# Performance work log

Measured on AMD Instinct MI355X. Metric: run time of the kernel, lower is better.

The kernel has to match this reference:

```python
import jax, jax.numpy as jnp
import numpy as np

D_MODEL = 1024
NUM_HEADS = 16
DEPTH = D_MODEL // NUM_HEADS


def setup_inputs() -> dict:
    key = jax.random.key(0)
    ks = jax.random.split(key, 6)
    B, S = 2, 2048
    scale = 1.0 / np.sqrt(D_MODEL)
    return {
        "q": jax.random.normal(ks[0], (B, S, D_MODEL), jnp.float32),
        "k": jax.random.normal(ks[1], (B, S, D_MODEL), jnp.float32),
        "v": jax.random.normal(ks[2], (B, S, D_MODEL), jnp.float32),
        "wq": jax.random.normal(ks[3], (D_MODEL, D_MODEL), jnp.float32) * scale,
        "wk": jax.random.normal(ks[4], (D_MODEL, D_MODEL), jnp.float32) * scale,
        "wv": jax.random.normal(ks[5], (D_MODEL, D_MODEL), jnp.float32) * scale,
    }


def reference(q, k, v, wq, wk, wv):
    B, S, _ = q.shape
    # Linear projections (nn.Linear: x @ W.T), then split heads -> [B,H,S,depth]
    def split(x):
        return x.reshape(B, -1, NUM_HEADS, DEPTH).transpose(0, 2, 1, 3)
    Q = split(q @ wq.T)
    K = split(k @ wk.T)
    V = split(v @ wv.T)
    scores = jnp.einsum("bhqd,bhkd->bhqk", Q, K) / np.sqrt(DEPTH).astype(np.float32)
    attn = jax.nn.softmax(scores, axis=-1)
    out = jnp.einsum("bhqk,bhkd->bhqd", attn, V)
    # merge heads; note: original forward never applies self.dense
    return out.transpose(0, 2, 1, 3).reshape(B, S, D_MODEL)
```

## Files before the change

kernel.cpp:

```cpp
#include <hip/hip_runtime.h>
#include <hip/hip_bf16.h>
#include <stdint.h>

#define B_SZ 2
#define S_LEN 2048
#define DM 1024
#define NH 16
#define DEPTH 64
#define M_ROWS (B_SZ * S_LEN)
#define SCALE_Q 0.1803368801111144f

typedef __attribute__((ext_vector_type(8))) short bf16x8;
typedef __attribute__((ext_vector_type(4))) float f32x4;
typedef __attribute__((ext_vector_type(16))) float f32x16;

__device__ __forceinline__ unsigned short f2bf(float x) {
    union { float f; unsigned u; } a; a.f = x;
    unsigned r = a.u + 0x7FFF + ((a.u >> 16) & 1);
    return (unsigned short)(r >> 16);
}

__device__ __forceinline__ void async_ld16(const unsigned short* g, void* l) {
    __builtin_amdgcn_global_load_lds(
        (const __attribute__((address_space(1))) void*)g,
        (__attribute__((address_space(3))) void*)l,
        16, 0, 0);
}


__global__ __launch_bounds__(256)
void convert_kernel(const float* __restrict__ q, const float* __restrict__ k,
                    const float* __restrict__ v, const float* __restrict__ wq,
                    const float* __restrict__ wk, const float* __restrict__ wv,
                    unsigned short* __restrict__ dst) {
    const int z = blockIdx.y;
    const float* src = (z == 0) ? q : (z == 1) ? k : (z == 2) ? v
                     : (z == 3) ? wq : (z == 4) ? wk : wv;
    const size_t n4  = (z < 3) ? ((size_t)M_ROWS * DM / 4) : ((size_t)DM * DM / 4);
    const size_t off = (z < 3) ? ((size_t)z * M_ROWS * DM)
                               : ((size_t)3 * M_ROWS * DM + (size_t)(z - 3) * DM * DM);
    unsigned short* d = dst + off;
    const size_t stride = (size_t)gridDim.x * blockDim.x;
    for (size_t i = (size_t)blockIdx.x * blockDim.x + threadIdx.x; i < n4; i += stride) {
        float4 x = ((const float4*)src)[i];
        ushort4 p;
        p.x = f2bf(x.x); p.y = f2bf(x.y); p.z = f2bf(x.z); p.w = f2bf(x.w);
        ((ushort4*)d)[i] = p;
    }
}

__global__ __launch_bounds__(256)
void proj_gemm3_kernel(const unsigned short* __restrict__ Xall,
                       const unsigned short* __restrict__ Wall,
                       unsigned short* __restrict__ Call) {
    __shared__ unsigned short As[128 * 64];
    __shared__ unsigned short Bs[128 * 64];

    const int z = blockIdx.z;
    const unsigned short* X = Xall + (size_t)z * M_ROWS * DM;
    const unsigned short* W = Wall + (size_t)z * DM * DM;
    unsigned short* C = Call + (size_t)z * M_ROWS * DM;

    const int tid  = threadIdx.x;
    const int wave = tid >> 6;
    const int lane = tid & 63;
    const int l32  = lane & 31;
    const int s    = lane >> 5;
    const int m0 = blockIdx.x * 128;
    const int n0 = blockIdx.y * 128;
    const int wm = (wave >> 1) * 64;
    const int wn = (wave & 1) * 64;

    const int r8 = lane >> 3;
    const int sc = (lane & 7) ^ r8;

    f32x16 acc[2][2];
#pragma unroll
    for (int mi = 0; mi < 2; ++mi)
#pragma unroll
        for (int ni = 0; ni < 2; ++ni)
#pragma unroll
            for (int r = 0; r < 16; ++r) acc[mi][ni][r] = 0.f;

    for (int k0 = 0; k0 < DM; k0 += 64) {
#pragma unroll
        for (int i = 0; i < 4; ++i) {
            const int r = i * 32 + wave * 8 + r8;
            async_ld16(X + (size_t)(m0 + r) * DM + k0 + sc * 8,
                       (char*)As + i * 4096 + wave * 1024);
            async_ld16(W + (size_t)(n0 + r) * DM + k0 + sc * 8,
                       (char*)Bs + i * 4096 + wave * 1024);
        }
        __syncthreads();

#pragma unroll
        for (int ch = 0; ch < 4; ++ch) {
            bf16x8 af[2], bfr[2];
#pragma unroll
            for (int mi = 0; mi < 2; ++mi) {
                const int row = wm + mi * 32 + l32;
                af[mi] = *(const bf16x8*)&As[row * 64 + (((2 * ch + s) ^ (row & 7)) * 8)];
            }
#pragma unroll
            for (int ni = 0; ni < 2; ++ni) {
                const int row = wn + ni * 32 + l32;
                bfr[ni] = *(const bf16x8*)&Bs[row * 64 + (((2 * ch + s) ^ (row & 7)) * 8)];
            }
#pragma unroll
            for (int mi = 0; mi < 2; ++mi)
#pragma unroll
                for (int ni = 0; ni < 2; ++ni)
                    acc[mi][ni] = __builtin_amdgcn_mfma_f32_32x32x16_bf16(
                        af[mi], bfr[ni], acc[mi][ni], 0, 0, 0);
        }
        __syncthreads();
    }

    const float scale = (z == 0) ? SCALE_Q : 1.0f;
#pragma unroll
    for (int mi = 0; mi < 2; ++mi)
#pragma unroll
        for (int ni = 0; ni < 2; ++ni)
#pragma unroll
            for (int r = 0; r < 16; ++r) {
                const int row = m0 + wm + mi * 32 + (r & 3) + 8 * (r >> 2) + 4 * s;
                const int col = n0 + wn + ni * 32 + l32;
                C[(size_t)row * DM + col] = f2bf(acc[mi][ni][r] * scale);
            }
}

__global__ __launch_bounds__(256)
void vtrans_kernel(const unsigned short* __restrict__ Vp,
                   unsigned short* __restrict__ Vt) {
    __shared__ unsigned short Ls[64 * 72];
    const int tr = blockIdx.x;
    const int h  = blockIdx.y;
    const int tid = threadIdx.x;

#pragma unroll
    for (int i = 0; i < 2; ++i) {
        const int id = i * 256 + tid;
        const int r = id >> 3, c = id & 7;
        bf16x8 v8 = *(const bf16x8*)&Vp[(size_t)(tr * 64 + r) * DM + h * 64 + c * 8];
        *(bf16x8*)&Ls[r * 72 + ((c ^ (r & 7)) * 8)] = v8;
    }
    __syncthreads();

    const int b = tr >> 5;
    const int col0 = (tr & 31) * 64;
#pragma unroll
    for (int i = 0; i < 2; ++i) {
        const int id = i * 256 + tid;
        const int d = id >> 3, c2 = id & 7;
        unsigned short tmp[8];
#pragma unroll
        for (int j = 0; j < 8; ++j) {
            const int cc = c2 * 8 + j;
            const int t = (cc >> 1) + ((cc & 1) << 5);
            tmp[j] = Ls[t * 72 + (((d >> 3) ^ (t & 7)) * 8) + (d & 7)];
        }
        *(bf16x8*)&Vt[(size_t)((b * NH + h) * DEPTH + d) * S_LEN + col0 + c2 * 8] =
            *(const bf16x8*)tmp;
    }
}

__global__ __launch_bounds__(256)
void attn3_kernel(const unsigned short* __restrict__ Qp,
                  const unsigned short* __restrict__ Kp,
                  const unsigned short* __restrict__ Vt,
                  float* __restrict__ out) {
    __shared__ unsigned short Ks[64 * 64];
    __shared__ unsigned short Vs[64 * 64];
    __shared__ unsigned short Ps[4 * 32 * 72];

    const int tid  = threadIdx.x;
    const int wave = tid >> 6;
    const int lane = tid & 63;
    const int l32  = lane & 31;
    const int s    = lane >> 5;
    const int q0 = blockIdx.x * 128;
    const int h  = blockIdx.y;
    const int b  = blockIdx.z;

    const int r8 = lane >> 3;
    const int sc = (lane & 7) ^ r8;

    const unsigned short* Kg = Kp + (size_t)(b * S_LEN) * DM + h * DEPTH;
    const unsigned short* Vg = Vt + (size_t)((b * NH + h) * DEPTH) * S_LEN;

    bf16x8 qf[4];
    {
        const unsigned short* p =
            Qp + (size_t)(b * S_LEN + q0 + wave * 32 + l32) * DM + h * DEPTH;
#pragma unroll
        for (int ch = 0; ch < 4; ++ch)
            qf[ch] = *(const bf16x8*)(p + ch * 16 + s * 8);
    }

    f32x16 oacc[2];
    float lacc[16];
#pragma unroll
    for (int d = 0; d < 2; ++d)
#pragma unroll
        for (int r = 0; r < 16; ++r) oacc[d][r] = 0.f;
#pragma unroll
    for (int r = 0; r < 16; ++r) lacc[r] = 0.f;

    unsigned short* PsW = &Ps[wave * 32 * 72];

    for (int t0 = 0; t0 < S_LEN; t0 += 64) {
#pragma unroll
        for (int i = 0; i < 2; ++i) {
            const int r = i * 32 + wave * 8 + r8;
            async_ld16(Kg + (size_t)(t0 + r) * DM + sc * 8,
                       (char*)Ks + i * 4096 + wave * 1024);
            async_ld16(Vg + (size_t)r * S_LEN + t0 + sc * 8,
                       (char*)Vs + i * 4096 + wave * 1024);
        }
        __syncthreads();

        f32x16 sacc[2];
#pragma unroll
        for (int tb = 0; tb < 2; ++tb) {
#pragma unroll
            for (int r = 0; r < 16; ++r) sacc[tb][r] = 0.f;
            const int trow = tb * 32 + l32;
#pragma unroll
            for (int ch = 0; ch < 4; ++ch) {
                bf16x8 kf = *(const bf16x8*)
                    &Ks[trow * 64 + (((2 * ch + s) ^ (trow & 7)) * 8)];
                sacc[tb] = __builtin_amdgcn_mfma_f32_32x32x16_bf16(
                    qf[ch], kf, sacc[tb], 0, 0, 0);
            }
        }

#pragma unroll
        for (int r = 0; r < 16; ++r) {
            const float p0 = __builtin_amdgcn_exp2f(sacc[0][r]);
            const float p1 = __builtin_amdgcn_exp2f(sacc[1][r]);
            union { float f; unsigned u; } a0, a1;
            a0.f = p0; a1.f = p1;
            union { unsigned u; float f; } t0f, t1f;
            t0f.u = a0.u & 0xFFFF0000u;
            t1f.u = a1.u & 0xFFFF0000u;
            lacc[r] += t0f.f + t1f.f;
            const unsigned pk = (a0.u >> 16) | (a1.u & 0xFFFF0000u);
            const int qrow = (r & 3) + 8 * (r >> 2) + 4 * s;
            *(unsigned*)&PsW[qrow * 72 + 2 * l32] = pk;
        }

        bf16x8 pf[4];
#pragma unroll
        for (int ch = 0; ch < 4; ++ch)
            pf[ch] = *(const bf16x8*)&PsW[l32 * 72 + ch * 16 + s * 8];
#pragma unroll
        for (int db = 0; db < 2; ++db) {
            const int drow = db * 32 + l32;
#pragma unroll
            for (int ch = 0; ch < 4; ++ch) {
                bf16x8 vf = *(const bf16x8*)
                    &Vs[drow * 64 + (((2 * ch + s) ^ (drow & 7)) * 8)];
                oacc[db] = __builtin_amdgcn_mfma_f32_32x32x16_bf16(
                    pf[ch], vf, oacc[db], 0, 0, 0);
            }
        }
        __syncthreads();
    }

#pragma unroll
    for (int r = 0; r < 16; ++r)
#pragma unroll
        for (int off = 1; off < 32; off <<= 1)
            lacc[r] += __shfl_xor(lacc[r], off, 64);

#pragma unroll
    for (int db = 0; db < 2; ++db)
#pragma unroll
        for (int r = 0; r < 16; ++r) {
            const int qrow = (r & 3) + 8 * (r >> 2) + 4 * s;
            const size_t row = (size_t)(b * S_LEN + q0 + wave * 32 + qrow);
            out[row * DM + h * DEPTH + db * 32 + l32] = oacc[db][r] / lacc[r];
        }
}

#define LDK 72

__global__ __launch_bounds__(256)
void proj_gemm_kernel(const float* __restrict__ q, const float* __restrict__ k,
                      const float* __restrict__ v, const float* __restrict__ wq,
                      const float* __restrict__ wk, const float* __restrict__ wv,
                      unsigned short* __restrict__ Qp, unsigned short* __restrict__ Kp,
                      unsigned short* __restrict__ Vp) {
    __shared__ unsigned short As[128 * LDK];
    __shared__ unsigned short Bs[128 * LDK];

    const int z = blockIdx.z;
    const float* __restrict__ X = (z == 0) ? q : (z == 1) ? k : v;
    const float* __restrict__ W = (z == 0) ? wq : (z == 1) ? wk : wv;
    unsigned short* __restrict__ C = (z == 0) ? Qp : (z == 1) ? Kp : Vp;

    const int tid  = threadIdx.x;
    const int wave = tid >> 6;
    const int lane = tid & 63;
    const int quad = lane >> 4;
    const int l16  = lane & 15;
    const int m0 = blockIdx.x * 128;
    const int n0 = blockIdx.y * 128;
    const int wm = (wave >> 1) * 64;
    const int wn = (wave & 1) * 64;

    f32x4 acc[4][4];
#pragma unroll
    for (int mt = 0; mt < 4; ++mt)
#pragma unroll
        for (int nt = 0; nt < 4; ++nt)
            acc[mt][nt] = (f32x4){0.f, 0.f, 0.f, 0.f};

    for (int k0 = 0; k0 < DM; k0 += 64) {
#pragma unroll
        for (int vv = 0; vv < 8; ++vv) {
            int vecid = tid + 256 * vv;
            int r  = vecid >> 4;
            int c4 = vecid & 15;
            const float4 xa = *(const float4*)&X[(size_t)(m0 + r) * DM + k0 + c4 * 4];
            ushort4 pa;
            pa.x = f2bf(xa.x); pa.y = f2bf(xa.y); pa.z = f2bf(xa.z); pa.w = f2bf(xa.w);
            *(ushort4*)&As[r * LDK + c4 * 4] = pa;
            const float4 xb = *(const float4*)&W[(size_t)(n0 + r) * DM + k0 + c4 * 4];
            ushort4 pb;
            pb.x = f2bf(xb.x); pb.y = f2bf(xb.y); pb.z = f2bf(xb.z); pb.w = f2bf(xb.w);
            *(ushort4*)&Bs[r * LDK + c4 * 4] = pb;
        }
        __syncthreads();

#pragma unroll
        for (int kc = 0; kc < 2; ++kc) {
            bf16x8 af[4], bfr[4];
#pragma unroll
            for (int mt = 0; mt < 4; ++mt)
                af[mt] = *(const bf16x8*)&As[(wm + mt * 16 + l16) * LDK + kc * 32 + quad * 8];
#pragma unroll
            for (int nt = 0; nt < 4; ++nt)
                bfr[nt] = *(const bf16x8*)&Bs[(wn + nt * 16 + l16) * LDK + kc * 32 + quad * 8];
#pragma unroll
            for (int mt = 0; mt < 4; ++mt)
#pragma unroll
                for (int nt = 0; nt < 4; ++nt)
                    acc[mt][nt] = __builtin_amdgcn_mfma_f32_16x16x32_bf16(
                        af[mt], bfr[nt], acc[mt][nt], 0, 0, 0);
        }
        __syncthreads();
    }

#pragma unroll
    for (int mt = 0; mt < 4; ++mt)
#pragma unroll
        for (int nt = 0; nt < 4; ++nt)
#pragma unroll
            for (int r = 0; r < 4; ++r) {
                int row = m0 + wm + mt * 16 + quad * 4 + r;
                int col = n0 + wn + nt * 16 + l16;
                C[(size_t)row * DM + col] = f2bf(acc[mt][nt][r]);
            }
}

__global__ __launch_bounds__(256)
void attn_kernel(const unsigned short* __restrict__ Qp,
                 const unsigned short* __restrict__ Kp,
                 const unsigned short* __restrict__ Vp,
                 float* __restrict__ out) {
    __shared__ unsigned short Ks[64 * LDK];
    __shared__ unsigned short Vtl[64 * LDK];
    __shared__ unsigned short Ps[4 * 16 * LDK];

    const int tid  = threadIdx.x;
    const int wave = tid >> 6;
    const int lane = tid & 63;
    const int quad = lane >> 4;
    const int l16  = lane & 15;
    const int q0 = blockIdx.x * 64;
    const int h  = blockIdx.y;
    const int b  = blockIdx.z;
    const int wbase = wave * 16 * LDK;

    bf16x8 qf[2];
    {
        size_t row = (size_t)b * S_LEN + q0 + wave * 16 + l16;
        const unsigned short* p = Qp + row * DM + h * DEPTH;
        qf[0] = *(const bf16x8*)(p + quad * 8);
        qf[1] = *(const bf16x8*)(p + 32 + quad * 8);
    }

    float m_i[4], l_i[4];
    f32x4 accO[4];
#pragma unroll
    for (int r = 0; r < 4; ++r) { m_i[r] = -1e30f; l_i[r] = 0.f; }
#pragma unroll
    for (int f = 0; f < 4; ++f) accO[f] = (f32x4){0.f, 0.f, 0.f, 0.f};

    for (int t0 = 0; t0 < S_LEN; t0 += 64) {
#pragma unroll
        for (int vv = 0; vv < 2; ++vv) {
            int vecid = tid + 256 * vv;
            int r  = vecid >> 3;
            int cv = vecid & 7;
            size_t grow = (size_t)(b * S_LEN + t0 + r) * DM + h * DEPTH + cv * 8;
            *(bf16x8*)&Ks[r * LDK + cv * 8] = *(const bf16x8*)(Kp + grow);
            bf16x8 vvv = *(const bf16x8*)(Vp + grow);
#pragma unroll
            for (int j = 0; j < 8; ++j)
                Vtl[(cv * 8 + j) * LDK + r] = ((const unsigned short*)&vvv)[j];
        }
        __syncthreads();

        f32x4 sc4[4];
#pragma unroll
        for (int nt = 0; nt < 4; ++nt) {
            f32x4 a = (f32x4){0.f, 0.f, 0.f, 0.f};
            bf16x8 kf0 = *(const bf16x8*)&Ks[(nt * 16 + l16) * LDK + quad * 8];
            bf16x8 kf1 = *(const bf16x8*)&Ks[(nt * 16 + l16) * LDK + 32 + quad * 8];
            a = __builtin_amdgcn_mfma_f32_16x16x32_bf16(qf[0], kf0, a, 0, 0, 0);
            a = __builtin_amdgcn_mfma_f32_16x16x32_bf16(qf[1], kf1, a, 0, 0, 0);
            sc4[nt] = a;
        }
#pragma unroll
        for (int nt = 0; nt < 4; ++nt)
#pragma unroll
            for (int r = 0; r < 4; ++r) sc4[nt][r] *= 0.125f;

#pragma unroll
        for (int r = 0; r < 4; ++r) {
            float mx = fmaxf(fmaxf(sc4[0][r], sc4[1][r]), fmaxf(sc4[2][r], sc4[3][r]));
#pragma unroll
            for (int off = 1; off < 16; off <<= 1)
                mx = fmaxf(mx, __shfl_xor(mx, off, 64));
            float mnew = fmaxf(m_i[r], mx);
            float alpha = __expf(m_i[r] - mnew);
            float rs = 0.f;
#pragma unroll
            for (int nt = 0; nt < 4; ++nt) {
                float p = __expf(sc4[nt][r] - mnew);
                sc4[nt][r] = p;
                rs += p;
            }
#pragma unroll
            for (int off = 1; off < 16; off <<= 1)
                rs += __shfl_xor(rs, off, 64);
            l_i[r] = l_i[r] * alpha + rs;
            m_i[r] = mnew;
#pragma unroll
            for (int f = 0; f < 4; ++f) accO[f][r] *= alpha;
        }

#pragma unroll
        for (int nt = 0; nt < 4; ++nt)
#pragma unroll
            for (int r = 0; r < 4; ++r)
                Ps[wbase + (quad * 4 + r) * LDK + nt * 16 + l16] = f2bf(sc4[nt][r]);
        __syncthreads();

        bf16x8 pf0 = *(const bf16x8*)&Ps[wbase + l16 * LDK + quad * 8];
        bf16x8 pf1 = *(const bf16x8*)&Ps[wbase + l16 * LDK + 32 + quad * 8];
#pragma unroll
        for (int f = 0; f < 4; ++f) {
            bf16x8 vf0 = *(const bf16x8*)&Vtl[(f * 16 + l16) * LDK + quad * 8];
            bf16x8 vf1 = *(const bf16x8*)&Vtl[(f * 16 + l16) * LDK + 32 + quad * 8];
            accO[f] = __builtin_amdgcn_mfma_f32_16x16x32_bf16(pf0, vf0, accO[f], 0, 0, 0);
            accO[f] = __builtin_amdgcn_mfma_f32_16x16x32_bf16(pf1, vf1, accO[f], 0, 0, 0);
        }
        __syncthreads();
    }

#pragma unroll
    for (int f = 0; f < 4; ++f)
#pragma unroll
        for (int r = 0; r < 4; ++r) {
            size_t row = (size_t)b * S_LEN + q0 + wave * 16 + quad * 4 + r;
            out[row * DM + h * DEPTH + f * 16 + l16] = accO[f][r] / l_i[r];
        }
}

extern "C" void kernel_launch(void* const* d_in, const int* in_sizes, int n_in,
                              void* d_out, int out_size, void* d_ws, size_t ws_size,
                              hipStream_t stream) {
    const float* q  = (const float*)d_in[0];
    const float* k  = (const float*)d_in[1];
    const float* v  = (const float*)d_in[2];
    const float* wq = (const float*)d_in[3];
    const float* wk = (const float*)d_in[4];
    const float* wv = (const float*)d_in[5];
    float* out = (float*)d_out;

    unsigned short* ws = (unsigned short*)d_ws;
    const size_t NPROJ = (size_t)M_ROWS * DM;
    const size_t NW    = (size_t)DM * DM;

    const size_t need = (3 * NPROJ + 3 * NW + 3 * NPROJ) * sizeof(unsigned short);

    if (ws_size >= need) {
        unsigned short* Xbf = ws;
        unsigned short* Wbf = ws + 3 * NPROJ;
        unsigned short* Cp  = ws + 3 * NPROJ + 3 * NW;
        unsigned short* Qp  = Cp;
        unsigned short* Kp  = Cp + NPROJ;
        unsigned short* Vp  = Cp + 2 * NPROJ;
        unsigned short* Vt  = ws;

        convert_kernel<<<dim3(256, 6), 256, 0, stream>>>(q, k, v, wq, wk, wv, Xbf);
        proj_gemm3_kernel<<<dim3(M_ROWS / 128, DM / 128, 3), 256, 0, stream>>>(Xbf, Wbf, Cp);
        vtrans_kernel<<<dim3(M_ROWS / 64, NH), 256, 0, stream>>>(Vp, Vt);
        attn3_kernel<<<dim3(S_LEN / 128, NH, B_SZ), 256, 0, stream>>>(Qp, Kp, Vt, out);
    } else {
        unsigned short* Qp = ws;
        unsigned short* Kp = ws + NPROJ;
        unsigned short* Vp = ws + 2 * NPROJ;
        proj_gemm_kernel<<<dim3(M_ROWS / 128, DM / 128, 3), 256, 0, stream>>>(
            q, k, v, wq, wk, wv, Qp, Kp, Vp);
        attn_kernel<<<dim3(S_LEN / 64, NH, B_SZ), 256, 0, stream>>>(Qp, Kp, Vp, out);
    }
}
```

Baseline: 203.1 us.

## Rewrite attention as single-wave blocks with double-buffered async K/V loads

Replaces the 4-wave attention kernel with a one-wave-per-block kernel that handles 64 queries, double-buffers K and V tiles in LDS through async global-to-LDS loads gated by waitcnt, and computes transposed score and output MFMAs (K·Q and V·P), so each lane holds one query row's sum and the full cross-lane reduction shrinks to a single shuffle. The output is staged through LDS for coalesced float4 stores, and the V-transpose kernel drops its key interleave to match the new P layout. The aim is to overlap global loads with MFMA work and remove block-wide barriers, at the cost of a larger LDS footprint per single-wave block and correctness relying on hand-written waitcnt encodings.

```diff
diff --git a/kernel.cpp b/kernel.cpp
--- a/kernel.cpp
+++ b/kernel.cpp
@@ -155,8 +155,7 @@
         unsigned short tmp[8];
 #pragma unroll
         for (int j = 0; j < 8; ++j) {
-            const int cc = c2 * 8 + j;
-            const int t = (cc >> 1) + ((cc & 1) << 5);
+            const int t = c2 * 8 + j;
             tmp[j] = Ls[t * 72 + (((d >> 3) ^ (t & 7)) * 8) + (d & 7)];
         }
         *(bf16x8*)&Vt[(size_t)((b * NH + h) * DEPTH + d) * S_LEN + col0 + c2 * 8] =
@@ -164,21 +163,20 @@
     }
 }
 
-__global__ __launch_bounds__(256)
-void attn3_kernel(const unsigned short* __restrict__ Qp,
+__global__ __launch_bounds__(64)
+void attn4_kernel(const unsigned short* __restrict__ Qp,
                   const unsigned short* __restrict__ Kp,
                   const unsigned short* __restrict__ Vt,
                   float* __restrict__ out) {
-    __shared__ unsigned short Ks[64 * 64];
-    __shared__ unsigned short Vs[64 * 64];
-    __shared__ unsigned short Ps[4 * 32 * 72];
-
-    const int tid  = threadIdx.x;
-    const int wave = tid >> 6;
-    const int lane = tid & 63;
+    __shared__ __align__(16) char smem[40960];
+    unsigned short* Ks = (unsigned short*)smem;
+    unsigned short* Vs = (unsigned short*)(smem + 16384);
+    unsigned short* Ps = (unsigned short*)(smem + 32768);
+
+    const int lane = threadIdx.x & 63;
     const int l32  = lane & 31;
     const int s    = lane >> 5;
-    const int q0 = blockIdx.x * 128;
+    const int q0 = blockIdx.x * 64;
     const int h  = blockIdx.y;
     const int b  = blockIdx.z;
 
@@ -188,99 +186,137 @@
     const unsigned short* Kg = Kp + (size_t)(b * S_LEN) * DM + h * DEPTH;
     const unsigned short* Vg = Vt + (size_t)((b * NH + h) * DEPTH) * S_LEN;
 
-    bf16x8 qf[4];
-    {
+    bf16x8 qf[2][4];
+#pragma unroll
+    for (int nq = 0; nq < 2; ++nq) {
         const unsigned short* p =
-            Qp + (size_t)(b * S_LEN + q0 + wave * 32 + l32) * DM + h * DEPTH;
+            Qp + (size_t)(b * S_LEN + q0 + nq * 32 + l32) * DM + h * DEPTH;
 #pragma unroll
         for (int ch = 0; ch < 4; ++ch)
-            qf[ch] = *(const bf16x8*)(p + ch * 16 + s * 8);
-    }
-
-    f32x16 oacc[2];
-    float lacc[16];
-#pragma unroll
-    for (int d = 0; d < 2; ++d)
-#pragma unroll
-        for (int r = 0; r < 16; ++r) oacc[d][r] = 0.f;
-#pragma unroll
-    for (int r = 0; r < 16; ++r) lacc[r] = 0.f;
-
-    unsigned short* PsW = &Ps[wave * 32 * 72];
-
-    for (int t0 = 0; t0 < S_LEN; t0 += 64) {
-#pragma unroll
-        for (int i = 0; i < 2; ++i) {
-            const int r = i * 32 + wave * 8 + r8;
-            async_ld16(Kg + (size_t)(t0 + r) * DM + sc * 8,
-                       (char*)Ks + i * 4096 + wave * 1024);
-            async_ld16(Vg + (size_t)r * S_LEN + t0 + sc * 8,
-                       (char*)Vs + i * 4096 + wave * 1024);
-        }
-        __syncthreads();
-
-        f32x16 sacc[2];
+            qf[nq][ch] = *(const bf16x8*)(p + ch * 16 + s * 8);
+    }
+
+    f32x16 oacc[2][2];
+    float lacc[2] = {0.f, 0.f};
+#pragma unroll
+    for (int db = 0; db < 2; ++db)
+#pragma unroll
+        for (int nq = 0; nq < 2; ++nq)
+#pragma unroll
+            for (int r = 0; r < 16; ++r) oacc[db][nq][r] = 0.f;
+
+#pragma unroll
+    for (int i = 0; i < 8; ++i) {
+        async_ld16(Kg + (size_t)(i * 8 + r8) * DM + sc * 8, (char*)Ks + i * 1024);
+        async_ld16(Vg + (size_t)(i * 8 + r8) * S_LEN + sc * 8, (char*)Vs + i * 1024);
+    }
+
+    for (int it = 0; it < S_LEN / 64; ++it) {
+        const int buf = it & 1;
+        if (it < S_LEN / 64 - 1) {
+            const int t1 = (it + 1) * 64;
+            char* kd = (char*)Ks + (buf ^ 1) * 8192;
+            char* vd = (char*)Vs + (buf ^ 1) * 8192;
+#pragma unroll
+            for (int i = 0; i < 8; ++i) {
+                async_ld16(Kg + (size_t)(t1 + i * 8 + r8) * DM + sc * 8,
+                           kd + i * 1024);
+                async_ld16(Vg + (size_t)(i * 8 + r8) * S_LEN + t1 + sc * 8,
+                           vd + i * 1024);
+            }
+            __builtin_amdgcn_s_waitcnt(0x4F70);
+        } else {
+            __builtin_amdgcn_s_waitcnt(0x0F70);
+        }
+        __builtin_amdgcn_sched_barrier(0);
+
+        const unsigned short* Kb = Ks + buf * 4096;
+        const unsigned short* Vb = Vs + buf * 4096;
+
 #pragma unroll
         for (int tb = 0; tb < 2; ++tb) {
-#pragma unroll
-            for (int r = 0; r < 16; ++r) sacc[tb][r] = 0.f;
+            f32x16 s0, s1;
+#pragma unroll
+            for (int r = 0; r < 16; ++r) { s0[r] = 0.f; s1[r] = 0.f; }
             const int trow = tb * 32 + l32;
 #pragma unroll
             for (int ch = 0; ch < 4; ++ch) {
                 bf16x8 kf = *(const bf16x8*)
-                    &Ks[trow * 64 + (((2 * ch + s) ^ (trow & 7)) * 8)];
-                sacc[tb] = __builtin_amdgcn_mfma_f32_32x32x16_bf16(
-                    qf[ch], kf, sacc[tb], 0, 0, 0);
-            }
-        }
-
-#pragma unroll
-        for (int r = 0; r < 16; ++r) {
-            const float p0 = __builtin_amdgcn_exp2f(sacc[0][r]);
-            const float p1 = __builtin_amdgcn_exp2f(sacc[1][r]);
-            union { float f; unsigned u; } a0, a1;
-            a0.f = p0; a1.f = p1;
-            union { unsigned u; float f; } t0f, t1f;
-            t0f.u = a0.u & 0xFFFF0000u;
-            t1f.u = a1.u & 0xFFFF0000u;
-            lacc[r] += t0f.f + t1f.f;
-            const unsigned pk = (a0.u >> 16) | (a1.u & 0xFFFF0000u);
-            const int qrow = (r & 3) + 8 * (r >> 2) + 4 * s;
-            *(unsigned*)&PsW[qrow * 72 + 2 * l32] = pk;
-        }
-
-        bf16x8 pf[4];
-#pragma unroll
-        for (int ch = 0; ch < 4; ++ch)
-            pf[ch] = *(const bf16x8*)&PsW[l32 * 72 + ch * 16 + s * 8];
-#pragma unroll
-        for (int db = 0; db < 2; ++db) {
-            const int drow = db * 32 + l32;
-#pragma unroll
-            for (int ch = 0; ch < 4; ++ch) {
+                    &Kb[trow * 64 + (((2 * ch + s) ^ (trow & 7)) * 8)];
+                s0 = __builtin_amdgcn_mfma_f32_32x32x16_bf16(kf, qf[0][ch], s0, 0, 0, 0);
+                s1 = __builtin_amdgcn_mfma_f32_32x32x16_bf16(kf, qf[1][ch], s1, 0, 0, 0);
+            }
+#pragma unroll
+            for (int nq = 0; nq < 2; ++nq) {
+                const int qq = nq * 32 + l32;
+#pragma unroll
+                for (int a = 0; a < 4; ++a) {
+                    union { float f; unsigned u; } e0, e1, e2, e3;
+                    e0.f = __builtin_amdgcn_exp2f(nq ? s1[4 * a + 0] : s0[4 * a + 0]);
+                    e1.f = __builtin_amdgcn_exp2f(nq ? s1[4 * a + 1] : s0[4 * a + 1]);
+                    e2.f = __builtin_amdgcn_exp2f(nq ? s1[4 * a + 2] : s0[4 * a + 2]);
+                    e3.f = __builtin_amdgcn_exp2f(nq ? s1[4 * a + 3] : s0[4 * a + 3]);
+                    union { unsigned u; float f; } t0, t1, t2, t3;
+                    t0.u = e0.u & 0xFFFF0000u; t1.u = e1.u & 0xFFFF0000u;
+                    t2.u = e2.u & 0xFFFF0000u; t3.u = e3.u & 0xFFFF0000u;
+                    lacc[nq] += (t0.f + t1.f) + (t2.f + t3.f);
+                    const int slot = (4 * tb + a) ^ (qq & 7);
+                    *(unsigned*)&Ps[qq * 64 + slot * 8 + 4 * s] =
+                        (e0.u >> 16) | (e1.u & 0xFFFF0000u);
+                    *(unsigned*)&Ps[qq * 64 + slot * 8 + 4 * s + 2] =
+                        (e2.u >> 16) | (e3.u & 0xFFFF0000u);
+                }
+            }
+        }
+        __builtin_amdgcn_sched_barrier(0);
+
+#pragma unroll
+        for (int ch = 0; ch < 4; ++ch) {
+            bf16x8 pf0 = *(const bf16x8*)
+                &Ps[l32 * 64 + (((2 * ch + s) ^ (l32 & 7)) * 8)];
+            bf16x8 pf1 = *(const bf16x8*)
+                &Ps[(32 + l32) * 64 + (((2 * ch + s) ^ (l32 & 7)) * 8)];
+#pragma unroll
+            for (int db = 0; db < 2; ++db) {
+                const int drow = db * 32 + l32;
                 bf16x8 vf = *(const bf16x8*)
-                    &Vs[drow * 64 + (((2 * ch + s) ^ (drow & 7)) * 8)];
-                oacc[db] = __builtin_amdgcn_mfma_f32_32x32x16_bf16(
-                    pf[ch], vf, oacc[db], 0, 0, 0);
-            }
-        }
-        __syncthreads();
-    }
-
-#pragma unroll
-    for (int r = 0; r < 16; ++r)
-#pragma unroll
-        for (int off = 1; off < 32; off <<= 1)
-            lacc[r] += __shfl_xor(lacc[r], off, 64);
-
+                    &Vb[drow * 64 + (((2 * ch + s) ^ (drow & 7)) * 8)];
+                oacc[db][0] = __builtin_amdgcn_mfma_f32_32x32x16_bf16(
+                    vf, pf0, oacc[db][0], 0, 0, 0);
+                oacc[db][1] = __builtin_amdgcn_mfma_f32_32x32x16_bf16(
+                    vf, pf1, oacc[db][1], 0, 0, 0);
+            }
+        }
+        __builtin_amdgcn_sched_barrier(0);
+    }
+
+    const float l0 = lacc[0] + __shfl_xor(lacc[0], 32, 64);
+    const float l1 = lacc[1] + __shfl_xor(lacc[1], 32, 64);
+    const float inv0 = 1.0f / l0, inv1 = 1.0f / l1;
+
+    __builtin_amdgcn_s_waitcnt(0xC07F);
+    __builtin_amdgcn_sched_barrier(0);
+    float* Of = (float*)(smem + 16384);
 #pragma unroll
     for (int db = 0; db < 2; ++db)
 #pragma unroll
-        for (int r = 0; r < 16; ++r) {
-            const int qrow = (r & 3) + 8 * (r >> 2) + 4 * s;
-            const size_t row = (size_t)(b * S_LEN + q0 + wave * 32 + qrow);
-            out[row * DM + h * DEPTH + db * 32 + l32] = oacc[db][r] / lacc[r];
-        }
+        for (int nq = 0; nq < 2; ++nq) {
+            const int qq = nq * 32 + l32;
+            const float inv = nq ? inv1 : inv0;
+#pragma unroll
+            for (int r = 0; r < 16; ++r) {
+                const int d = db * 32 + (r & 3) + 8 * (r >> 2) + 4 * s;
+                Of[qq * 68 + d] = oacc[db][nq][r] * inv;
+            }
+        }
+    __builtin_amdgcn_sched_barrier(0);
+#pragma unroll
+    for (int i = 0; i < 16; ++i) {
+        const int row = i * 4 + (lane >> 4);
+        const int c4 = lane & 15;
+        float4 v = *(const float4*)&Of[row * 68 + c4 * 4];
+        *(float4*)&out[(size_t)(b * S_LEN + q0 + row) * DM + h * DEPTH + c4 * 4] = v;
+    }
 }
 
 #define LDK 72
@@ -509,7 +545,7 @@
         convert_kernel<<<dim3(256, 6), 256, 0, stream>>>(q, k, v, wq, wk, wv, Xbf);
         proj_gemm3_kernel<<<dim3(M_ROWS / 128, DM / 128, 3), 256, 0, stream>>>(Xbf, Wbf, Cp);
         vtrans_kernel<<<dim3(M_ROWS / 64, NH), 256, 0, stream>>>(Vp, Vt);
-        attn3_kernel<<<dim3(S_LEN / 128, NH, B_SZ), 256, 0, stream>>>(Qp, Kp, Vt, out);
+        attn4_kernel<<<dim3(S_LEN / 64, NH, B_SZ), 64, 0, stream>>>(Qp, Kp, Vt, out);
     } else {
         unsigned short* Qp = ws;
         unsigned short* Kp = ws + NPROJ;
```

Result: slower. 213.5 us (+5.1%).
